# Performance work log

Measured on AMD Instinct MI355X. Metric: run time of the kernel, lower is better.

The kernel has to match this reference:

```python
import jax, jax.numpy as jnp
import numpy as np

INPUT_DIM = 2048
CLASSES = 1000
BATCH = 8192


def setup_inputs() -> dict:
    key = jax.random.key(0)
    kx, ky, kwx, kbx, kwy, kby = jax.random.split(key, 6)
    s_in = 1.0 / np.sqrt(INPUT_DIM)
    return {
        "x": jax.random.normal(kx, (BATCH, INPUT_DIM), dtype=jnp.float32),
        "y": jax.random.normal(ky, (BATCH, INPUT_DIM), dtype=jnp.float32),
        "Wx": jax.random.uniform(kwx, (CLASSES, INPUT_DIM), jnp.float32, -s_in, s_in),
        "bx": jax.random.uniform(kbx, (CLASSES,), jnp.float32, -s_in, s_in),
        "Wy": jax.random.uniform(kwy, (CLASSES, INPUT_DIM), jnp.float32, -s_in, s_in),
        "by": jax.random.uniform(kby, (CLASSES,), jnp.float32, -s_in, s_in),
    }


def _ds_combin_two(alpha1, alpha2, classes):
    # alpha1, alpha2: [B, C] Dirichlet params
    S1 = jnp.sum(alpha1, axis=1, keepdims=True)  # [B,1]
    S2 = jnp.sum(alpha2, axis=1, keepdims=True)
    b1 = (alpha1 - 1.0) / S1                      # belief masses [B,C]
    b2 = (alpha2 - 1.0) / S2
    u1 = classes / S1                             # uncertainty [B,1]
    u2 = classes / S2
    # bb_sum = sum_{i,j} b1_i b2_j = (sum b1)(sum b2); bb_diag = sum_i b1_i b2_i
    bb_sum = jnp.sum(b1, axis=1) * jnp.sum(b2, axis=1)   # [B]
    bb_diag = jnp.sum(b1 * b2, axis=1)                    # [B]
    C = (bb_sum - bb_diag)[:, None]                       # conflict [B,1]
    denom = 1.0 - C
    b_a = (b1 * b2 + b1 * u2 + b2 * u1) / denom           # [B,C]
    u_a = (u1 * u2) / denom                               # [B,1]
    S_a = classes / u_a                                   # [B,1]
    return b_a * S_a + 1.0                                # alpha_a [B,C]


def reference(x, y, Wx, bx, Wy, by):
    out_x = x @ Wx.T + bx                 # [B,C]
    out_y = y @ Wy.T + by
    alpha_x = jax.nn.softplus(out_x) + 1.0
    alpha_y = jax.nn.softplus(out_y) + 1.0
    alpha_a = _ds_combin_two(alpha_x, alpha_y, CLASSES)
    return (alpha_a, alpha_x, alpha_y)
```

## Files before the change

kernel.cpp:

```cpp
#include <hip/hip_runtime.h>
#include <hip/hip_bf16.h>
#include <math.h>

#define BATCH_N 8192
#define K_DIM   2048
#define CLS     1000

typedef __attribute__((ext_vector_type(8))) short short8;
typedef __attribute__((ext_vector_type(8))) unsigned short ushort8;
typedef __attribute__((ext_vector_type(4))) float floatx4;

static __device__ __forceinline__ float softplus_fast(float z) {
    return fmaxf(z, 0.f) + __logf(1.f + __expf(-fabsf(z)));
}

static __device__ __forceinline__ ushort f2bfr(float f) {
    return __hip_bfloat16_raw(__float2bfloat16(f)).x;
}

#define BARX  __builtin_amdgcn_s_barrier()
#define LGKM0 asm volatile("s_waitcnt lgkmcnt(0)" ::: "memory")
#define SB0   __builtin_amdgcn_sched_barrier(0)
#define PRIO1 __builtin_amdgcn_s_setprio(1)
#define PRIO0 __builtin_amdgcn_s_setprio(0)

constexpr int NT = K_DIM / 32;


__global__ __launch_bounds__(1024, 2)
void gemm_fused(const float* __restrict__ Xa, const float* __restrict__ Xb,
                const float* __restrict__ Wa, const float* __restrict__ Wb,
                const float* __restrict__ biasa, const float* __restrict__ biasb,
                float* __restrict__ outa, float* __restrict__ outb)
{
    int flat = blockIdx.x + 4 * (blockIdx.y + 32 * blockIdx.z);
    int sw   = (flat & 7) * 32 + (flat >> 3);
    const int bx = sw & 3, by = (sw >> 2) & 31, bz = sw >> 7;

    const float* A    = bz ? Xb : Xa;
    const float* B    = bz ? Wb : Wa;
    const float* bias = bz ? biasb : biasa;
    float* out        = bz ? outb : outa;

    __shared__ ushort As[2][256 * 32];
    __shared__ ushort Bs[2][256 * 32];

    const int tid  = threadIdx.x;
    const int lane = tid & 63;
    const int wid  = tid >> 6;
    const int wr = wid >> 2, wc = wid & 3;
    const int fr = lane & 15, fg = lane >> 4;
    const int brow = by * 256;
    const int bcol = bx * 256;

    size_t a_g, b_g;
    int    l_of;
    {
        int q = tid;
        int p = q >> 3, c8 = q & 7, c8l = c8 ^ (p & 7);
        int r = 2 * p + (c8l >> 2);
        int k = (c8l & 3) * 8;
        a_g = (size_t)(brow + r) * K_DIM + k;
        int wrow = bcol + r; if (wrow >= CLS) wrow = CLS - 1;
        b_g = (size_t)wrow * K_DIM + k;
        l_of = q * 8;
    }

    int afoff[4], bfoff[4];
#pragma unroll
    for (int m = 0; m < 4; ++m) {
        int row = wr * 64 + m * 16 + fr;
        int p = row >> 1;
        int c = (((row & 1) << 2) | fg) ^ (p & 7);
        afoff[m] = (p * 8 + c) * 8;
    }
#pragma unroll
    for (int n = 0; n < 4; ++n) {
        int row = wc * 64 + n * 16 + fr;
        int p = row >> 1;
        int c = (((row & 1) << 2) | fg) ^ (p & 7);
        bfoff[n] = (p * 8 + c) * 8;
    }

    floatx4 acc[4][4];
#pragma unroll
    for (int m = 0; m < 4; ++m)
#pragma unroll
        for (int n = 0; n < 4; ++n)
            acc[m][n] = (floatx4){0.f, 0.f, 0.f, 0.f};

    float4 ga[2], gb[2];

#define LOADT(t_) {                                                           \
    const size_t kb_ = (size_t)(t_) * 32;                                     \
    ga[0] = *(const float4*)(A + a_g + kb_);                                  \
    ga[1] = *(const float4*)(A + a_g + kb_ + 4);                              \
    gb[0] = *(const float4*)(B + b_g + kb_);                                  \
    gb[1] = *(const float4*)(B + b_g + kb_ + 4);                              \
}

#define CVTW(sl_) {                                                           \
    ushort8 ta, tb;                                                           \
    _Pragma("unroll")                                                         \
    for (int j = 0; j < 4; ++j) {                                             \
        ta[j]     = f2bfr(((const float*)&ga[0])[j]);                         \
        ta[j + 4] = f2bfr(((const float*)&ga[1])[j]);                         \
        tb[j]     = f2bfr(((const float*)&gb[0])[j]);                         \
        tb[j + 4] = f2bfr(((const float*)&gb[1])[j]);                         \
    }                                                                         \
    *(ushort8*)&As[sl_][l_of] = ta;                                           \
    *(ushort8*)&Bs[sl_][l_of] = tb;                                           \
}

    LOADT(0)
    CVTW(0)
    LOADT(1)
    SB0; LGKM0; BARX; SB0;

#pragma unroll 1
    for (int t = 0; t < NT; ++t) {
        const ushort* asl = &As[t & 1][0];
        const ushort* bsl = &Bs[t & 1][0];
        short8 af[4], bf[4];
#pragma unroll
        for (int m = 0; m < 4; ++m) af[m] = *(const short8*)(asl + afoff[m]);
#pragma unroll
        for (int n = 0; n < 4; ++n) bf[n] = *(const short8*)(bsl + bfoff[n]);

        PRIO1;
#pragma unroll
        for (int m = 0; m < 4; ++m)
#pragma unroll
            for (int n = 0; n < 4; ++n)
                acc[m][n] = __builtin_amdgcn_mfma_f32_16x16x32_bf16(
                    af[m], bf[n], acc[m][n], 0, 0, 0);
        PRIO0;

        if (t + 1 < NT) CVTW((t + 1) & 1)
        if (t + 2 < NT) LOADT(t + 2)
        SB0; LGKM0; BARX; SB0;
    }

#pragma unroll
    for (int n = 0; n < 4; ++n) {
        int col = bcol + wc * 64 + n * 16 + fr;
        if (col >= CLS) continue;
        float bv = bias[col];
#pragma unroll
        for (int m = 0; m < 4; ++m) {
#pragma unroll
            for (int j = 0; j < 4; ++j) {
                int row = brow + wr * 64 + m * 16 + fg * 4 + j;
                float z = acc[m][n][j] + bv;
                out[(size_t)row * CLS + col] = softplus_fast(z) + 1.f;
            }
        }
    }
}


__global__ __launch_bounds__(256)
void ds_combine(const float* __restrict__ AX, const float* __restrict__ AY,
                float* __restrict__ out)
{
    const int row = blockIdx.x * 4 + (threadIdx.x >> 6);
    const int l = threadIdx.x & 63;
    const float* ax = AX + (size_t)row * CLS;
    const float* ay = AY + (size_t)row * CLS;

    float4 vx[4], vy[4];
    float sx = 0.f, sy = 0.f, sp = 0.f;
#pragma unroll
    for (int c = 0; c < 4; ++c) {
        int idx = l + c * 64;
        if (idx < CLS / 4) {
            vx[c] = *(const float4*)(ax + idx * 4);
            vy[c] = *(const float4*)(ay + idx * 4);
            const float* px = (const float*)&vx[c];
            const float* py = (const float*)&vy[c];
#pragma unroll
            for (int j = 0; j < 4; ++j) {
                sx += px[j]; sy += py[j];
                sp += (px[j] - 1.f) * (py[j] - 1.f);
            }
        }
    }
#pragma unroll
    for (int off = 1; off < 64; off <<= 1) {
        sx += __shfl_xor(sx, off);
        sy += __shfl_xor(sy, off);
        sp += __shfl_xor(sp, off);
    }
    const float S1 = sx, S2 = sy, P = sp;
    const float i1 = 1.f / S1, i2 = 1.f / S2;
    const float u1 = (float)CLS * i1, u2 = (float)CLS * i2;
    const float sb1 = (S1 - (float)CLS) * i1;
    const float sb2 = (S2 - (float)CLS) * i2;
    const float conf = sb1 * sb2 - P * i1 * i2;
    const float denom = 1.f - conf;
    const float idenom = 1.f / denom;
    const float Sa = (float)CLS * denom / (u1 * u2);

#pragma unroll
    for (int c = 0; c < 4; ++c) {
        int idx = l + c * 64;
        if (idx < CLS / 4) {
            float4 vo;
            const float* px = (const float*)&vx[c];
            const float* py = (const float*)&vy[c];
            float* po = (float*)&vo;
#pragma unroll
            for (int j = 0; j < 4; ++j) {
                float b1 = (px[j] - 1.f) * i1;
                float b2 = (py[j] - 1.f) * i2;
                float ba = (b1 * b2 + b1 * u2 + b2 * u1) * idenom;
                po[j] = ba * Sa + 1.f;
            }
            *(float4*)(out + (size_t)row * CLS + idx * 4) = vo;
        }
    }
}

extern "C" void kernel_launch(void* const* d_in, const int* in_sizes, int n_in,
                              void* d_out, int out_size, void* d_ws, size_t ws_size,
                              hipStream_t stream) {
    const float* x  = (const float*)d_in[0];
    const float* y  = (const float*)d_in[1];
    const float* Wx = (const float*)d_in[2];
    const float* bx = (const float*)d_in[3];
    const float* Wy = (const float*)d_in[4];
    const float* by = (const float*)d_in[5];
    float* out = (float*)d_out;
    float* ax = out + (size_t)BATCH_N * CLS;
    float* ay = ax  + (size_t)BATCH_N * CLS;

    gemm_fused<<<dim3(4, 32, 2), 1024, 0, stream>>>(
        x, y, Wx, Wy, bx, by, ax, ay);
    ds_combine<<<BATCH_N / 4, 256, 0, stream>>>(ax, ay, out);
}
```

Measured before the change: 111.1 us.

## Use four LDS stages and barrier once per two k-tiles

Grows the shared-memory staging buffers from two to four slots and unrolls the main loop by two. Each half-step computes one tile, converts the next-but-one tile into LDS and issues the following global load, so only one workgroup barrier is needed per pair of tiles. The goal is to halve barrier and lgkmcnt wait stalls in the 1024-thread GEMM. In exchange, LDS use doubles to 128KB, so only one workgroup fits per CU. With 256 workgroups on this grid, that is likely roughly one per CU already.

New measurement: 118.9 us. +7.1%, slower.

```diff
diff --git a/kernel.cpp b/kernel.cpp
--- a/kernel.cpp
+++ b/kernel.cpp
@@ -42,8 +42,8 @@
     const float* bias = bz ? biasb : biasa;
     float* out        = bz ? outb : outa;
 
-    __shared__ ushort As[2][256 * 32];
-    __shared__ ushort Bs[2][256 * 32];
+    __shared__ ushort As[4][256 * 32];
+    __shared__ ushort Bs[4][256 * 32];
 
     const int tid  = threadIdx.x;
     const int lane = tid & 63;
@@ -112,32 +112,40 @@
     *(ushort8*)&Bs[sl_][l_of] = tb;                                           \
 }
 
+#define COMPUTE(t_) {                                                         \
+    const ushort* asl = &As[(t_) & 3][0];                                     \
+    const ushort* bsl = &Bs[(t_) & 3][0];                                     \
+    short8 af[4], bf[4];                                                      \
+    _Pragma("unroll")                                                         \
+    for (int m = 0; m < 4; ++m) af[m] = *(const short8*)(asl + afoff[m]);     \
+    _Pragma("unroll")                                                         \
+    for (int n = 0; n < 4; ++n) bf[n] = *(const short8*)(bsl + bfoff[n]);     \
+    PRIO1;                                                                    \
+    _Pragma("unroll")                                                         \
+    for (int m = 0; m < 4; ++m)                                               \
+        _Pragma("unroll")                                                     \
+        for (int n = 0; n < 4; ++n)                                           \
+            acc[m][n] = __builtin_amdgcn_mfma_f32_16x16x32_bf16(              \
+                af[m], bf[n], acc[m][n], 0, 0, 0);                            \
+    PRIO0;                                                                    \
+}
+
     LOADT(0)
     CVTW(0)
     LOADT(1)
+    CVTW(1)
+    LOADT(2)
     SB0; LGKM0; BARX; SB0;
 
 #pragma unroll 1
-    for (int t = 0; t < NT; ++t) {
-        const ushort* asl = &As[t & 1][0];
-        const ushort* bsl = &Bs[t & 1][0];
-        short8 af[4], bf[4];
-#pragma unroll
-        for (int m = 0; m < 4; ++m) af[m] = *(const short8*)(asl + afoff[m]);
-#pragma unroll
-        for (int n = 0; n < 4; ++n) bf[n] = *(const short8*)(bsl + bfoff[n]);
-
-        PRIO1;
-#pragma unroll
-        for (int m = 0; m < 4; ++m)
-#pragma unroll
-            for (int n = 0; n < 4; ++n)
-                acc[m][n] = __builtin_amdgcn_mfma_f32_16x16x32_bf16(
-                    af[m], bf[n], acc[m][n], 0, 0, 0);
-        PRIO0;
-
-        if (t + 1 < NT) CVTW((t + 1) & 1)
-        if (t + 2 < NT) LOADT(t + 2)
+    for (int s = 0; s < NT / 2; ++s) {
+        const int t0 = 2 * s, t1 = 2 * s + 1;
+        COMPUTE(t0)
+        if (t0 + 2 < NT) CVTW((t0 + 2) & 3)
+        if (t0 + 3 < NT) LOADT(t0 + 3)
+        COMPUTE(t1)
+        if (t1 + 2 < NT) CVTW((t1 + 2) & 3)
+        if (t1 + 3 < NT) LOADT(t1 + 3)
         SB0; LGKM0; BARX; SB0;
     }
 
```
